# Performance work log

Measured on AMD Instinct MI355X. Metric: run time of the kernel, lower is better.

The kernel has to match this reference:

```python
import jax, jax.numpy as jnp
import numpy as np
import math

B, S, E, H, L, FF = 32, 512, 256, 8, 4, 1024
DH = E // H
EPS = 1e-5


def layernorm(x):
    # nn.LayerNorm(elementwise_affine=False)
    m = jnp.mean(x, axis=-1, keepdims=True)
    v = jnp.mean((x - m) ** 2, axis=-1, keepdims=True)
    return (x - m) / jnp.sqrt(v + EPS)


def make_pos_embedding(e):
    vals = [math.sin(1 / 10000 ** ((i - 1) / e)) if i % 2 == 1
            else math.cos(i / 10000 ** ((i - 1) / e)) for i in range(e)]
    return jnp.asarray(np.array(vals, dtype=np.float32))


def setup_inputs() -> dict:
    key = jax.random.key(0)
    ks = jax.random.split(key, 8)
    sc = 0.02
    x = jax.random.normal(ks[0], (B, S, E), dtype=jnp.float32)
    Wq = jax.random.normal(ks[1], (L, H, DH, DH), dtype=jnp.float32) * sc
    Wk = jax.random.normal(ks[2], (L, H, DH, DH), dtype=jnp.float32) * sc
    Wv = jax.random.normal(ks[3], (L, H, DH, DH), dtype=jnp.float32) * sc
    W1 = jax.random.normal(ks[4], (L, E, FF), dtype=jnp.float32) * sc
    b1 = jnp.zeros((L, FF), dtype=jnp.float32)
    W2 = jax.random.normal(ks[5], (L, FF, E), dtype=jnp.float32) * sc
    b2 = jnp.zeros((L, E), dtype=jnp.float32)
    pos = make_pos_embedding(E)
    return {"x": x, "pos": pos, "Wq": Wq, "Wk": Wk, "Wv": Wv,
            "W1": W1, "b1": b1, "W2": W2, "b2": b2}


def encoder_layer(x, wq, wk, wv, w1, bb1, w2, bb2):
    xn = layernorm(x)
    xh = xn.reshape(B, S, H, DH)  # split embedding into per-head chunks
    q = jnp.einsum('bshd,hde->bhse', xh, wq)
    k = jnp.einsum('bshd,hde->bhse', xh, wk)
    v = jnp.einsum('bshd,hde->bhse', xh, wv)
    scores = jnp.einsum('bhsd,bhtd->bhst', q, k) / jnp.sqrt(jnp.float32(DH))
    a = jax.nn.softmax(scores, axis=-1)
    o = jnp.einsum('bhst,bhtd->bhsd', a, v)
    mha = o.transpose(0, 2, 1, 3).reshape(B, S, E)  # concat heads
    res = mha + x
    rn = layernorm(res)
    ffn = jax.nn.gelu(rn @ w1 + bb1, approximate=False) @ w2 + bb2
    return ffn + res


def reference(x, pos, Wq, Wk, Wv, W1, b1, W2, b2):
    h = x + pos  # fixed sinusoidal positional embedding
    for l in range(L):
        h = encoder_layer(h, Wq[l], Wk[l], Wv[l], W1[l], b1[l], W2[l], b2[l])
    return h
```

## Files before the change

### kernel.cpp

```cpp
#include <hip/hip_runtime.h>
#include <math.h>

#define BB   32
#define SS   512
#define EE   256
#define HH   8
#define LL   4
#define FFD  1024
#define DHD  32

constexpr float LN_EPS = 1e-5f;
constexpr int   NBSE   = BB * SS * EE;

typedef float  f32x4  __attribute__((ext_vector_type(4)));
typedef __bf16 bf16;
typedef __bf16 bf16x4 __attribute__((ext_vector_type(4)));
typedef __bf16 bf16x8 __attribute__((ext_vector_type(8)));

__device__ __forceinline__ void glds16(const bf16* g, bf16* l) {
    __builtin_amdgcn_global_load_lds(
        (const __attribute__((address_space(1))) void*)g,
        (__attribute__((address_space(3))) void*)l,
        16, 0, 0);
}

__device__ __forceinline__ float gelu_f(float x) {
    float u = x * x;
    float t = 1.5957691216057308f * x * (1.0f + 0.044715f * u);
    return x / (1.0f + __expf(-t));
}

__global__ __launch_bounds__(256) void k_cvt_t(const float* __restrict__ in,
                                               bf16* __restrict__ out,
                                               int K, int N) {
    __shared__ float tile[32][33];
    in  += (size_t)blockIdx.z * K * N;
    out += (size_t)blockIdx.z * K * N;
    int n0 = blockIdx.x * 32, k0 = blockIdx.y * 32;
    int tx = threadIdx.x & 31, ty = threadIdx.x >> 5;
    #pragma unroll
    for (int i = 0; i < 32; i += 8)
        tile[ty + i][tx] = in[(size_t)(k0 + ty + i) * N + n0 + tx];
    __syncthreads();
    #pragma unroll
    for (int i = 0; i < 32; i += 8)
        out[(size_t)(n0 + ty + i) * K + k0 + tx] = (bf16)tile[tx][ty + i];
}

__global__ __launch_bounds__(256) void k_cvt_qkv(const float* __restrict__ Wq,
                                                 const float* __restrict__ Wk,
                                                 const float* __restrict__ Wv,
                                                 bf16* __restrict__ Wqt,
                                                 bf16* __restrict__ Wkt,
                                                 bf16* __restrict__ Wvt) {
    __shared__ float tile[32][33];
    int lh = blockIdx.x;
    int z  = blockIdx.y;
    const float* in = (z == 0 ? Wq : z == 1 ? Wk : Wv) + (size_t)lh * 1024;
    bf16* out       = (z == 0 ? Wqt : z == 1 ? Wkt : Wvt) + (size_t)lh * 1024;
    float scale = (z == 0) ? 0.17677669529663687f : 1.0f;
    int tx = threadIdx.x & 31, ty = threadIdx.x >> 5;
    #pragma unroll
    for (int i = 0; i < 32; i += 8)
        tile[ty + i][tx] = in[(ty + i) * 32 + tx];
    __syncthreads();
    #pragma unroll
    for (int i = 0; i < 32; i += 8)
        out[(ty + i) * 32 + tx] = (bf16)(tile[tx][ty + i] * scale);
}

template <bool ADDPOS>
__global__ __launch_bounds__(256) void k_lnqkv(const float* __restrict__ xin,
                                               const float* __restrict__ pos,
                                               float* __restrict__ hout,
                                               const bf16* __restrict__ Wqt,
                                               const bf16* __restrict__ Wkt,
                                               const bf16* __restrict__ Wvt,
                                               bf16* __restrict__ qb,
                                               bf16* __restrict__ kb,
                                               bf16* __restrict__ vb) {
    __shared__ __attribute__((aligned(16))) bf16 Xs[64 * 264];
    int b = blockIdx.x, s0 = blockIdx.y * 64;
    int tid = threadIdx.x, w = tid >> 6, lane = tid & 63;
    size_t rowoff = ((size_t)(b * SS + s0 + w * 16)) * EE + lane * 4;
    const float* hb = xin + rowoff;
    float4 pv;
    if (ADDPOS) pv = *(const float4*)(pos + lane * 4);
    float4 xr[16];
    #pragma unroll
    for (int i = 0; i < 16; i++)
        xr[i] = *(const float4*)(hb + (size_t)i * EE);
    if (ADDPOS) {
        #pragma unroll
        for (int i = 0; i < 16; i++) {
            xr[i].x += pv.x; xr[i].y += pv.y; xr[i].z += pv.z; xr[i].w += pv.w;
            *(float4*)(hout + rowoff + (size_t)i * EE) = xr[i];
        }
    }
    #pragma unroll
    for (int i = 0; i < 16; i++) {
        float4 v4 = xr[i];
        float sum = v4.x + v4.y + v4.z + v4.w;
        #pragma unroll
        for (int m = 1; m <= 32; m <<= 1) sum += __shfl_xor(sum, m, 64);
        float mean = sum * (1.0f / EE);
        float dx = v4.x - mean, dy = v4.y - mean, dz = v4.z - mean, dw = v4.w - mean;
        float ss = dx * dx + dy * dy + dz * dz + dw * dw;
        #pragma unroll
        for (int m = 1; m <= 32; m <<= 1) ss += __shfl_xor(ss, m, 64);
        float rstd = rsqrtf(ss * (1.0f / EE) + LN_EPS);
        bf16x4 o4 = { (bf16)(dx * rstd), (bf16)(dy * rstd), (bf16)(dz * rstd), (bf16)(dw * rstd) };
        *(bf16x4*)&Xs[(w * 16 + i) * 264 + lane * 4] = o4;
    }
    __syncthreads();
    int col = lane & 15, quad = lane >> 4;
    #pragma unroll
    for (int h = 0; h < HH; h++) {
        bf16x8 a = *(const bf16x8*)&Xs[(w * 16 + col) * 264 + h * 32 + quad * 8];
        size_t base = ((size_t)((b * HH + h) * SS) + s0 + w * 16) * DHD;
        #pragma unroll
        for (int nt = 0; nt < 2; nt++) {
            int e = nt * 16 + col;
            bf16x8 bq  = *(const bf16x8*)(Wqt + (h * 32 + e) * 32 + quad * 8);
            bf16x8 bk2 = *(const bf16x8*)(Wkt + (h * 32 + e) * 32 + quad * 8);
            bf16x8 bv2 = *(const bf16x8*)(Wvt + (h * 32 + e) * 32 + quad * 8);
            f32x4 z = {0.f, 0.f, 0.f, 0.f};
            f32x4 cq = __builtin_amdgcn_mfma_f32_16x16x32_bf16(a, bq, z, 0, 0, 0);
            f32x4 ck = __builtin_amdgcn_mfma_f32_16x16x32_bf16(a, bk2, z, 0, 0, 0);
            f32x4 cv = __builtin_amdgcn_mfma_f32_16x16x32_bf16(a, bv2, z, 0, 0, 0);
            #pragma unroll
            for (int r = 0; r < 4; r++) {
                qb[base + (quad * 4 + r) * DHD + e] = (bf16)cq[r];
                kb[base + (quad * 4 + r) * DHD + e] = (bf16)ck[r];
            }
            bf16x4 vv = { (bf16)cv[0], (bf16)cv[1], (bf16)cv[2], (bf16)cv[3] };
            *(bf16x4*)&vb[(((size_t)(b * HH + h)) * DHD + e) * SS + s0 + w * 16 + quad * 4] = vv;
        }
    }
}

#define ATT_LDK 40
#define ATT_LDV 264
#define ATT_LDP 36
__global__ __launch_bounds__(256) void k_attn(const bf16* __restrict__ Q,
                                              const bf16* __restrict__ K,
                                              const bf16* __restrict__ VT,
                                              bf16* __restrict__ O) {
    __shared__ __attribute__((aligned(16))) bf16 Ks[256 * ATT_LDK];
    __shared__ __attribute__((aligned(16))) bf16 Vs[32 * ATT_LDV];
    __shared__ __attribute__((aligned(16))) bf16 Ps[4][16 * ATT_LDP];
    int bh = blockIdx.x;
    int q0 = blockIdx.y * 128;
    int tid = threadIdx.x;
    int w = tid >> 6, lane = tid & 63;
    int col = lane & 15, quad = lane >> 4;
    bf16x8 aq[2];
    #pragma unroll
    for (int sub = 0; sub < 2; sub++)
        aq[sub] = *(const bf16x8*)(Q + ((size_t)(bh * SS + q0 + sub * 64 + w * 16 + col)) * DHD + quad * 8);
    float lr[2] = {0.f, 0.f};
    f32x4 oacc[2][2] = {};
    int ksr = tid >> 2, ksc = (tid & 3) * 8;
    int vd  = tid >> 5, vso = (tid & 31) * 8;
    for (int ph = 0; ph < 2; ph++) {
        int t00 = ph * 256;
        __syncthreads();
        #pragma unroll
        for (int it = 0; it < 4; it++) {
            int rl = it * 64 + ksr;
            *(bf16x8*)&Ks[rl * ATT_LDK + ksc] =
                *(const bf16x8*)(K + ((size_t)(bh * SS + t00 + rl)) * DHD + ksc);
        }
        #pragma unroll
        for (int it = 0; it < 4; it++) {
            int d = it * 8 + vd;
            *(bf16x8*)&Vs[d * ATT_LDV + vso] =
                *(const bf16x8*)(VT + (((size_t)bh * DHD + d) * SS) + t00 + vso);
        }
        __syncthreads();
        #pragma unroll
        for (int i = 0; i < 8; i++) {
            bf16x8 bk[2], bv[2];
            #pragma unroll
            for (int nt = 0; nt < 2; nt++) {
                bk[nt] = *(const bf16x8*)&Ks[(i * 32 + nt * 16 + col) * ATT_LDK + quad * 8];
                bv[nt] = *(const bf16x8*)&Vs[(nt * 16 + col) * ATT_LDV + i * 32 + quad * 8];
            }
            __builtin_amdgcn_s_setprio(1);
            #pragma unroll
            for (int sub = 0; sub < 2; sub++) {
                #pragma unroll
                for (int nt = 0; nt < 2; nt++) {
                    f32x4 z = {0.f, 0.f, 0.f, 0.f};
                    f32x4 st = __builtin_amdgcn_mfma_f32_16x16x32_bf16(bk[nt], aq[sub], z, 0, 0, 0);
                    bf16x4 p4;
                    #pragma unroll
                    for (int r = 0; r < 4; r++) {
                        float p = __expf(st[r]);
                        lr[sub] += p;
                        p4[r] = (bf16)p;
                    }
                    *(bf16x4*)&Ps[w][col * ATT_LDP + nt * 16 + quad * 4] = p4;
                }
                bf16x4 apl = *(const bf16x4*)&Ps[w][col * ATT_LDP + quad * 8];
                bf16x4 aph = *(const bf16x4*)&Ps[w][col * ATT_LDP + quad * 8 + 4];
                bf16x8 ap;
                ap[0] = apl[0]; ap[1] = apl[1]; ap[2] = apl[2]; ap[3] = apl[3];
                ap[4] = aph[0]; ap[5] = aph[1]; ap[6] = aph[2]; ap[7] = aph[3];
                #pragma unroll
                for (int nt = 0; nt < 2; nt++)
                    oacc[sub][nt] = __builtin_amdgcn_mfma_f32_16x16x32_bf16(ap, bv[nt], oacc[sub][nt], 0, 0, 0);
            }
            __builtin_amdgcn_s_setprio(0);
        }
    }
    int b = bh >> 3, hh = bh & 7;
    #pragma unroll
    for (int sub = 0; sub < 2; sub++) {
        float ls = lr[sub];
        ls += __shfl_xor(ls, 16, 64);
        ls += __shfl_xor(ls, 32, 64);
        #pragma unroll
        for (int r = 0; r < 4; r++) {
            float lrow = __shfl(ls, quad * 4 + r, 64);
            float inv = 1.0f / lrow;
            int row = q0 + sub * 64 + w * 16 + quad * 4 + r;
            size_t ob = ((size_t)(b * SS + row)) * EE + hh * 32;
            O[ob + col]      = (bf16)(oacc[sub][0][r] * inv);
            O[ob + 16 + col] = (bf16)(oacc[sub][1][r] * inv);
        }
    }
}

__global__ __launch_bounds__(256, 3) void k_gemm1f(const bf16* __restrict__ ob,
                                                   const float* __restrict__ hb,
                                                   const bf16* __restrict__ Bt,
                                                   const float* __restrict__ bias,
                                                   bf16* __restrict__ C) {
    __shared__ __attribute__((aligned(16))) bf16 As[64 * 256];
    __shared__ __attribute__((aligned(16))) bf16 Bs[256 * 32];
    int tid = threadIdx.x, w = tid >> 6, lane = tid & 63;
    int col = lane & 15, quad = lane >> 4;
    int row0 = blockIdx.x * 64, col0 = blockIdx.y * 256;

    #pragma unroll 4
    for (int rr = 0; rr < 16; rr++) {
        int r = w * 16 + rr;
        size_t g = (size_t)(row0 + r) * EE + lane * 4;
        float4 h4 = *(const float4*)(hb + g);
        bf16x4 o4 = *(const bf16x4*)(ob + g);
        float v0 = h4.x + (float)o4[0], v1 = h4.y + (float)o4[1];
        float v2 = h4.z + (float)o4[2], v3 = h4.w + (float)o4[3];
        float s1 = v0 + v1 + v2 + v3;
        float s2 = v0 * v0 + v1 * v1 + v2 * v2 + v3 * v3;
        #pragma unroll
        for (int m = 1; m <= 32; m <<= 1) {
            s1 += __shfl_xor(s1, m, 64);
            s2 += __shfl_xor(s2, m, 64);
        }
        float mean = s1 * (1.0f / EE);
        float rstd = rsqrtf(s2 * (1.0f / EE) - mean * mean + LN_EPS);
        bf16x4 a4 = { (bf16)((v0 - mean) * rstd), (bf16)((v1 - mean) * rstd),
                      (bf16)((v2 - mean) * rstd), (bf16)((v3 - mean) * rstd) };
        *(bf16x4*)&As[r * 256 + ((lane * 4) ^ ((r & 7) << 3))] = a4;
    }

    int bc = lane >> 2;
    int bp = lane & 3;
    f32x4 acc[4][4] = {};
    for (int k0 = 0; k0 < EE; k0 += 32) {
        __syncthreads();
        #pragma unroll
        for (int i = 0; i < 4; i++) {
            int c = (w * 4 + i) * 16 + bc;
            glds16(Bt + (size_t)(col0 + c) * EE + k0 + ((bp ^ (c & 3)) * 8),
                   &Bs[(w * 4 + i) * 16 * 32]);
        }
        __syncthreads();
        bf16x8 af[4], bf_[4];
        #pragma unroll
        for (int mt = 0; mt < 4; mt++) {
            int r = mt * 16 + col;
            af[mt] = *(const bf16x8*)&As[r * 256 + ((k0 + quad * 8) ^ ((r & 7) << 3))];
        }
        #pragma unroll
        for (int nt = 0; nt < 4; nt++) {
            int c = w * 64 + nt * 16 + col;
            bf_[nt] = *(const bf16x8*)&Bs[c * 32 + ((quad * 8) ^ ((c & 3) << 3))];
        }
        #pragma unroll
        for (int mt = 0; mt < 4; mt++)
            #pragma unroll
            for (int nt = 0; nt < 4; nt++)
                acc[mt][nt] = __builtin_amdgcn_mfma_f32_16x16x32_bf16(bf_[nt], af[mt], acc[mt][nt], 0, 0, 0);
    }
    #pragma unroll
    for (int mt = 0; mt < 4; mt++) {
        int row = row0 + mt * 16 + col;
        #pragma unroll
        for (int nt = 0; nt < 4; nt++) {
            int cc = col0 + w * 64 + nt * 16 + quad * 4;
            float4 b4 = *(const float4*)&bias[cc];
            bf16x4 ov;
            ov[0] = (bf16)gelu_f(acc[mt][nt][0] + b4.x);
            ov[1] = (bf16)gelu_f(acc[mt][nt][1] + b4.y);
            ov[2] = (bf16)gelu_f(acc[mt][nt][2] + b4.z);
            ov[3] = (bf16)gelu_f(acc[mt][nt][3] + b4.w);
            *(bf16x4*)&C[(size_t)row * FFD + cc] = ov;
        }
    }
}

__global__ __launch_bounds__(256) void k_gemm2(const bf16* __restrict__ A,
                                               const bf16* __restrict__ Bt,
                                               const float* __restrict__ bias,
                                               const bf16* __restrict__ ob,
                                               const float* __restrict__ hb,
                                               float* __restrict__ Cf) {
    __shared__ __attribute__((aligned(16))) bf16 As[128 * 64];
    __shared__ __attribute__((aligned(16))) bf16 Bs[64 * 64];
    int tid = threadIdx.x, w = tid >> 6, lane = tid & 63;
    int col = lane & 15, quad = lane >> 4;
    int row0 = blockIdx.x * 128, col0 = blockIdx.y * 64;
    int srow = lane >> 3;
    int spos = lane & 7;
    f32x4 acc[2][4] = {};
    for (int k0 = 0; k0 < FFD; k0 += 64) {
        __syncthreads();
        #pragma unroll
        for (int i = 0; i < 4; i++) {
            int r = (w * 4 + i) * 8 + srow;
            glds16(A + (size_t)(row0 + r) * FFD + k0 + ((spos ^ (r & 7)) * 8),
                   &As[(w * 4 + i) * 8 * 64]);
        }
        #pragma unroll
        for (int i = 0; i < 2; i++) {
            int r = (w * 2 + i) * 8 + srow;
            glds16(Bt + (size_t)(col0 + r) * FFD + k0 + ((spos ^ (r & 7)) * 8),
                   &Bs[(w * 2 + i) * 8 * 64]);
        }
        __syncthreads();
        bf16x8 af[2][2], bf_[4][2];
        #pragma unroll
        for (int mt = 0; mt < 2; mt++) {
            int r = w * 32 + mt * 16 + col;
            #pragma unroll
            for (int kk = 0; kk < 2; kk++)
                af[mt][kk] = *(const bf16x8*)&As[r * 64 + ((kk * 32 + quad * 8) ^ ((r & 7) << 3))];
        }
        #pragma unroll
        for (int nt = 0; nt < 4; nt++) {
            int r = nt * 16 + col;
            #pragma unroll
            for (int kk = 0; kk < 2; kk++)
                bf_[nt][kk] = *(const bf16x8*)&Bs[r * 64 + ((kk * 32 + quad * 8) ^ ((r & 7) << 3))];
        }
        #pragma unroll
        for (int kk = 0; kk < 2; kk++)
            #pragma unroll
            for (int mt = 0; mt < 2; mt++)
                #pragma unroll
                for (int nt = 0; nt < 4; nt++)
                    acc[mt][nt] = __builtin_amdgcn_mfma_f32_16x16x32_bf16(bf_[nt][kk], af[mt][kk], acc[mt][nt], 0, 0, 0);
    }
    #pragma unroll
    for (int mt = 0; mt < 2; mt++) {
        int row = row0 + w * 32 + mt * 16 + col;
        #pragma unroll
        for (int nt = 0; nt < 4; nt++) {
            int cc = col0 + nt * 16 + quad * 4;
            float4 b4 = *(const float4*)&bias[cc];
            float4 h4 = *(const float4*)&hb[(size_t)row * EE + cc];
            bf16x4 o4 = *(const bf16x4*)&ob[(size_t)row * EE + cc];
            float4 out;
            out.x = acc[mt][nt][0] + b4.x + h4.x + (float)o4[0];
            out.y = acc[mt][nt][1] + b4.y + h4.y + (float)o4[1];
            out.z = acc[mt][nt][2] + b4.z + h4.z + (float)o4[2];
            out.w = acc[mt][nt][3] + b4.w + h4.w + (float)o4[3];
            *(float4*)&Cf[(size_t)row * EE + cc] = out;
        }
    }
}

extern "C" void kernel_launch(void* const* d_in, const int* in_sizes, int n_in,
                              void* d_out, int out_size, void* d_ws, size_t ws_size,
                              hipStream_t stream) {
    (void)in_sizes; (void)n_in; (void)out_size; (void)ws_size;
    const float* x   = (const float*)d_in[0];
    const float* pos = (const float*)d_in[1];
    const float* Wq  = (const float*)d_in[2];
    const float* Wk  = (const float*)d_in[3];
    const float* Wv  = (const float*)d_in[4];
    const float* W1  = (const float*)d_in[5];
    const float* b1  = (const float*)d_in[6];
    const float* W2  = (const float*)d_in[7];
    const float* b2  = (const float*)d_in[8];

    float* ws = (float*)d_ws;
    size_t N = (size_t)NBSE;
    float* h  = ws;
    bf16* ob  = (bf16*)(ws + N);
    bf16* qb  = (bf16*)(ws + 2 * N);
    bf16* kb  = qb + N;
    bf16* vb  = kb + N;
    bf16* ffb = (bf16*)(ws + 2 * N);
    bf16* W1t = (bf16*)(ws + 4 * N);
    bf16* W2t = W1t + (size_t)LL * EE * FFD;
    bf16* Wqt = W2t + (size_t)LL * EE * FFD;
    bf16* Wkt = Wqt + (size_t)LL * HH * DHD * DHD;
    bf16* Wvt = Wkt + (size_t)LL * HH * DHD * DHD;

    k_cvt_t<<<dim3(FFD / 32, EE / 32, LL), 256, 0, stream>>>(W1, W1t, EE, FFD);
    k_cvt_t<<<dim3(EE / 32, FFD / 32, LL), 256, 0, stream>>>(W2, W2t, FFD, EE);
    k_cvt_qkv<<<dim3(LL * HH, 3), 256, 0, stream>>>(Wq, Wk, Wv, Wqt, Wkt, Wvt);
    for (int l = 0; l < LL; l++) {
        if (l == 0)
            k_lnqkv<true><<<dim3(BB, SS / 64), 256, 0, stream>>>(
                x, pos, h, Wqt, Wkt, Wvt, qb, kb, vb);
        else
            k_lnqkv<false><<<dim3(BB, SS / 64), 256, 0, stream>>>(
                h, nullptr, nullptr,
                Wqt + (size_t)l * HH * DHD * DHD, Wkt + (size_t)l * HH * DHD * DHD,
                Wvt + (size_t)l * HH * DHD * DHD, qb, kb, vb);
        k_attn<<<dim3(BB * HH, SS / 128), 256, 0, stream>>>(qb, kb, vb, ob);
        k_gemm1f<<<dim3(BB * SS / 64, FFD / 256), 256, 0, stream>>>(
            ob, h, W1t + (size_t)l * FFD * EE, b1 + (size_t)l * FFD, ffb);
        float* outp = (l == LL - 1) ? (float*)d_out : h;
        k_gemm2<<<dim3(BB * SS / 128, EE / 64), 256, 0, stream>>>(
            ffb, W2t + (size_t)l * EE * FFD, b2 + (size_t)l * EE, ob, h, outp);
    }
}
```

Before: 443.1 us.

## Double-buffer GEMM tiles, prefetch attention K/V, merge weight prep, vectorize QKV stores

```diff
diff --git a/kernel.cpp b/kernel.cpp
--- a/kernel.cpp
+++ b/kernel.cpp
@@ -30,43 +30,50 @@
     return x / (1.0f + __expf(-t));
 }
 
-__global__ __launch_bounds__(256) void k_cvt_t(const float* __restrict__ in,
-                                               bf16* __restrict__ out,
-                                               int K, int N) {
+__global__ __launch_bounds__(256) void k_prep(const float* __restrict__ W1,
+                                              const float* __restrict__ W2,
+                                              const float* __restrict__ Wq,
+                                              const float* __restrict__ Wk,
+                                              const float* __restrict__ Wv,
+                                              bf16* __restrict__ W1t,
+                                              bf16* __restrict__ W2t,
+                                              bf16* __restrict__ Wqt,
+                                              bf16* __restrict__ Wkt,
+                                              bf16* __restrict__ Wvt) {
     __shared__ float tile[32][33];
-    in  += (size_t)blockIdx.z * K * N;
-    out += (size_t)blockIdx.z * K * N;
-    int n0 = blockIdx.x * 32, k0 = blockIdx.y * 32;
+    int bid = blockIdx.x;
     int tx = threadIdx.x & 31, ty = threadIdx.x >> 5;
-    #pragma unroll
-    for (int i = 0; i < 32; i += 8)
-        tile[ty + i][tx] = in[(size_t)(k0 + ty + i) * N + n0 + tx];
-    __syncthreads();
-    #pragma unroll
-    for (int i = 0; i < 32; i += 8)
-        out[(size_t)(n0 + ty + i) * K + k0 + tx] = (bf16)tile[tx][ty + i];
-}
-
-__global__ __launch_bounds__(256) void k_cvt_qkv(const float* __restrict__ Wq,
-                                                 const float* __restrict__ Wk,
-                                                 const float* __restrict__ Wv,
-                                                 bf16* __restrict__ Wqt,
-                                                 bf16* __restrict__ Wkt,
-                                                 bf16* __restrict__ Wvt) {
-    __shared__ float tile[32][33];
-    int lh = blockIdx.x;
-    int z  = blockIdx.y;
-    const float* in = (z == 0 ? Wq : z == 1 ? Wk : Wv) + (size_t)lh * 1024;
-    bf16* out       = (z == 0 ? Wqt : z == 1 ? Wkt : Wvt) + (size_t)lh * 1024;
-    float scale = (z == 0) ? 0.17677669529663687f : 1.0f;
-    int tx = threadIdx.x & 31, ty = threadIdx.x >> 5;
-    #pragma unroll
-    for (int i = 0; i < 32; i += 8)
-        tile[ty + i][tx] = in[(ty + i) * 32 + tx];
-    __syncthreads();
-    #pragma unroll
-    for (int i = 0; i < 32; i += 8)
-        out[(ty + i) * 32 + tx] = (bf16)(tile[tx][ty + i] * scale);
+    if (bid < 2048) {
+        bool isw2 = bid >= 1024;
+        int id = isw2 ? bid - 1024 : bid;
+        int K = isw2 ? FFD : EE, N = isw2 ? EE : FFD;
+        int l = id >> 8, rem = id & 255;
+        int n0, k0;
+        if (isw2) { n0 = (rem & 7) * 32;  k0 = (rem >> 3) * 32; }
+        else      { n0 = (rem & 31) * 32; k0 = (rem >> 5) * 32; }
+        const float* in = (isw2 ? W2 : W1) + (size_t)l * K * N;
+        bf16* out       = (isw2 ? W2t : W1t) + (size_t)l * K * N;
+        #pragma unroll
+        for (int i = 0; i < 32; i += 8)
+            tile[ty + i][tx] = in[(size_t)(k0 + ty + i) * N + n0 + tx];
+        __syncthreads();
+        #pragma unroll
+        for (int i = 0; i < 32; i += 8)
+            out[(size_t)(n0 + ty + i) * K + k0 + tx] = (bf16)tile[tx][ty + i];
+    } else {
+        int id = bid - 2048;
+        int lh = id & 31, z = id >> 5;
+        const float* in = (z == 0 ? Wq : z == 1 ? Wk : Wv) + (size_t)lh * 1024;
+        bf16* out       = (z == 0 ? Wqt : z == 1 ? Wkt : Wvt) + (size_t)lh * 1024;
+        float scale = (z == 0) ? 0.17677669529663687f : 1.0f;
+        #pragma unroll
+        for (int i = 0; i < 32; i += 8)
+            tile[ty + i][tx] = in[(ty + i) * 32 + tx];
+        __syncthreads();
+        #pragma unroll
+        for (int i = 0; i < 32; i += 8)
+            out[(ty + i) * 32 + tx] = (bf16)(tile[tx][ty + i] * scale);
+    }
 }
 
 template <bool ADDPOS>
@@ -125,14 +132,14 @@
             bf16x8 bk2 = *(const bf16x8*)(Wkt + (h * 32 + e) * 32 + quad * 8);
             bf16x8 bv2 = *(const bf16x8*)(Wvt + (h * 32 + e) * 32 + quad * 8);
             f32x4 z = {0.f, 0.f, 0.f, 0.f};
-            f32x4 cq = __builtin_amdgcn_mfma_f32_16x16x32_bf16(a, bq, z, 0, 0, 0);
-            f32x4 ck = __builtin_amdgcn_mfma_f32_16x16x32_bf16(a, bk2, z, 0, 0, 0);
+            f32x4 cq = __builtin_amdgcn_mfma_f32_16x16x32_bf16(bq, a, z, 0, 0, 0);
+            f32x4 ck = __builtin_amdgcn_mfma_f32_16x16x32_bf16(bk2, a, z, 0, 0, 0);
             f32x4 cv = __builtin_amdgcn_mfma_f32_16x16x32_bf16(a, bv2, z, 0, 0, 0);
-            #pragma unroll
-            for (int r = 0; r < 4; r++) {
-                qb[base + (quad * 4 + r) * DHD + e] = (bf16)cq[r];
-                kb[base + (quad * 4 + r) * DHD + e] = (bf16)ck[r];
-            }
+            bf16x4 q4 = { (bf16)cq[0], (bf16)cq[1], (bf16)cq[2], (bf16)cq[3] };
+            bf16x4 k4 = { (bf16)ck[0], (bf16)ck[1], (bf16)ck[2], (bf16)ck[3] };
+            size_t tb = base + (size_t)col * DHD + nt * 16 + quad * 4;
+            *(bf16x4*)&qb[tb] = q4;
+            *(bf16x4*)&kb[tb] = k4;
             bf16x4 vv = { (bf16)cv[0], (bf16)cv[1], (bf16)cv[2], (bf16)cv[3] };
             *(bf16x4*)&vb[(((size_t)(b * HH + h)) * DHD + e) * SS + s0 + w * 16 + quad * 4] = vv;
         }
@@ -162,20 +169,25 @@
     f32x4 oacc[2][2] = {};
     int ksr = tid >> 2, ksc = (tid & 3) * 8;
     int vd  = tid >> 5, vso = (tid & 31) * 8;
+    bf16x8 kr[4], vr[4];
+    #pragma unroll
+    for (int it = 0; it < 4; it++) {
+        kr[it] = *(const bf16x8*)(K + ((size_t)(bh * SS + it * 64 + ksr)) * DHD + ksc);
+        vr[it] = *(const bf16x8*)(VT + (((size_t)bh * DHD + it * 8 + vd) * SS) + vso);
+    }
     for (int ph = 0; ph < 2; ph++) {
-        int t00 = ph * 256;
         __syncthreads();
         #pragma unroll
         for (int it = 0; it < 4; it++) {
-            int rl = it * 64 + ksr;
-            *(bf16x8*)&Ks[rl * ATT_LDK + ksc] =
-                *(const bf16x8*)(K + ((size_t)(bh * SS + t00 + rl)) * DHD + ksc);
-        }
-        #pragma unroll
-        for (int it = 0; it < 4; it++) {
-            int d = it * 8 + vd;
-            *(bf16x8*)&Vs[d * ATT_LDV + vso] =
-                *(const bf16x8*)(VT + (((size_t)bh * DHD + d) * SS) + t00 + vso);
+            *(bf16x8*)&Ks[(it * 64 + ksr) * ATT_LDK + ksc] = kr[it];
+            *(bf16x8*)&Vs[(it * 8 + vd) * ATT_LDV + vso] = vr[it];
+        }
+        if (ph == 0) {
+            #pragma unroll
+            for (int it = 0; it < 4; it++) {
+                kr[it] = *(const bf16x8*)(K + ((size_t)(bh * SS + 256 + it * 64 + ksr)) * DHD + ksc);
+                vr[it] = *(const bf16x8*)(VT + (((size_t)bh * DHD + it * 8 + vd) * SS) + 256 + vso);
+            }
         }
         __syncthreads();
         #pragma unroll
@@ -232,13 +244,13 @@
     }
 }
 
-__global__ __launch_bounds__(256, 3) void k_gemm1f(const bf16* __restrict__ ob,
+__global__ __launch_bounds__(256, 2) void k_gemm1f(const bf16* __restrict__ ob,
                                                    const float* __restrict__ hb,
                                                    const bf16* __restrict__ Bt,
                                                    const float* __restrict__ bias,
                                                    bf16* __restrict__ C) {
     __shared__ __attribute__((aligned(16))) bf16 As[64 * 256];
-    __shared__ __attribute__((aligned(16))) bf16 Bs[256 * 32];
+    __shared__ __attribute__((aligned(16))) bf16 Bs[2][256 * 32];
     int tid = threadIdx.x, w = tid >> 6, lane = tid & 63;
     int col = lane & 15, quad = lane >> 4;
     int row0 = blockIdx.x * 64, col0 = blockIdx.y * 256;
@@ -267,16 +279,26 @@
 
     int bc = lane >> 2;
     int bp = lane & 3;
-    f32x4 acc[4][4] = {};
-    for (int k0 = 0; k0 < EE; k0 += 32) {
-        __syncthreads();
+    auto stageB = [&](int buf, int k0) {
         #pragma unroll
         for (int i = 0; i < 4; i++) {
             int c = (w * 4 + i) * 16 + bc;
             glds16(Bt + (size_t)(col0 + c) * EE + k0 + ((bp ^ (c & 3)) * 8),
-                   &Bs[(w * 4 + i) * 16 * 32]);
-        }
-        __syncthreads();
+                   &Bs[buf][(w * 4 + i) * 16 * 32]);
+        }
+    };
+    asm volatile("s_waitcnt lgkmcnt(0)" ::: "memory");
+    stageB(0, 0);
+    f32x4 acc[4][4] = {};
+    for (int t = 0; t < 8; t++) {
+        if (t < 7) {
+            stageB((t + 1) & 1, (t + 1) * 32);
+            asm volatile("s_waitcnt vmcnt(4)" ::: "memory");
+        } else {
+            asm volatile("s_waitcnt vmcnt(0)" ::: "memory");
+        }
+        __builtin_amdgcn_s_barrier();
+        int k0 = t * 32, buf = t & 1;
         bf16x8 af[4], bf_[4];
         #pragma unroll
         for (int mt = 0; mt < 4; mt++) {
@@ -286,13 +308,14 @@
         #pragma unroll
         for (int nt = 0; nt < 4; nt++) {
             int c = w * 64 + nt * 16 + col;
-            bf_[nt] = *(const bf16x8*)&Bs[c * 32 + ((quad * 8) ^ ((c & 3) << 3))];
+            bf_[nt] = *(const bf16x8*)&Bs[buf][c * 32 + ((quad * 8) ^ ((c & 3) << 3))];
         }
         #pragma unroll
         for (int mt = 0; mt < 4; mt++)
             #pragma unroll
             for (int nt = 0; nt < 4; nt++)
                 acc[mt][nt] = __builtin_amdgcn_mfma_f32_16x16x32_bf16(bf_[nt], af[mt], acc[mt][nt], 0, 0, 0);
+        __builtin_amdgcn_s_barrier();
     }
     #pragma unroll
     for (int mt = 0; mt < 4; mt++) {
@@ -311,49 +334,58 @@
     }
 }
 
-__global__ __launch_bounds__(256) void k_gemm2(const bf16* __restrict__ A,
-                                               const bf16* __restrict__ Bt,
-                                               const float* __restrict__ bias,
-                                               const bf16* __restrict__ ob,
-                                               const float* __restrict__ hb,
-                                               float* __restrict__ Cf) {
-    __shared__ __attribute__((aligned(16))) bf16 As[128 * 64];
-    __shared__ __attribute__((aligned(16))) bf16 Bs[64 * 64];
+__global__ __launch_bounds__(256, 3) void k_gemm2(const bf16* __restrict__ A,
+                                                  const bf16* __restrict__ Bt,
+                                                  const float* __restrict__ bias,
+                                                  const bf16* __restrict__ ob,
+                                                  const float* __restrict__ hb,
+                                                  float* __restrict__ Cf) {
+    __shared__ __attribute__((aligned(16))) bf16 As[2][128 * 64];
+    __shared__ __attribute__((aligned(16))) bf16 Bs[2][64 * 64];
     int tid = threadIdx.x, w = tid >> 6, lane = tid & 63;
     int col = lane & 15, quad = lane >> 4;
     int row0 = blockIdx.x * 128, col0 = blockIdx.y * 64;
     int srow = lane >> 3;
     int spos = lane & 7;
-    f32x4 acc[2][4] = {};
-    for (int k0 = 0; k0 < FFD; k0 += 64) {
-        __syncthreads();
+    auto stageAB = [&](int buf, int k0) {
         #pragma unroll
         for (int i = 0; i < 4; i++) {
             int r = (w * 4 + i) * 8 + srow;
             glds16(A + (size_t)(row0 + r) * FFD + k0 + ((spos ^ (r & 7)) * 8),
-                   &As[(w * 4 + i) * 8 * 64]);
+                   &As[buf][(w * 4 + i) * 8 * 64]);
         }
         #pragma unroll
         for (int i = 0; i < 2; i++) {
             int r = (w * 2 + i) * 8 + srow;
             glds16(Bt + (size_t)(col0 + r) * FFD + k0 + ((spos ^ (r & 7)) * 8),
-                   &Bs[(w * 2 + i) * 8 * 64]);
-        }
-        __syncthreads();
+                   &Bs[buf][(w * 2 + i) * 8 * 64]);
+        }
+    };
+    stageAB(0, 0);
+    f32x4 acc[2][4] = {};
+    for (int t = 0; t < 16; t++) {
+        if (t < 15) {
+            stageAB((t + 1) & 1, (t + 1) * 64);
+            asm volatile("s_waitcnt vmcnt(6)" ::: "memory");
+        } else {
+            asm volatile("s_waitcnt vmcnt(0)" ::: "memory");
+        }
+        __builtin_amdgcn_s_barrier();
+        int buf = t & 1;
         bf16x8 af[2][2], bf_[4][2];
         #pragma unroll
         for (int mt = 0; mt < 2; mt++) {
             int r = w * 32 + mt * 16 + col;
             #pragma unroll
             for (int kk = 0; kk < 2; kk++)
-                af[mt][kk] = *(const bf16x8*)&As[r * 64 + ((kk * 32 + quad * 8) ^ ((r & 7) << 3))];
+                af[mt][kk] = *(const bf16x8*)&As[buf][r * 64 + ((kk * 32 + quad * 8) ^ ((r & 7) << 3))];
         }
         #pragma unroll
         for (int nt = 0; nt < 4; nt++) {
             int r = nt * 16 + col;
             #pragma unroll
             for (int kk = 0; kk < 2; kk++)
-                bf_[nt][kk] = *(const bf16x8*)&Bs[r * 64 + ((kk * 32 + quad * 8) ^ ((r & 7) << 3))];
+                bf_[nt][kk] = *(const bf16x8*)&Bs[buf][r * 64 + ((kk * 32 + quad * 8) ^ ((r & 7) << 3))];
         }
         #pragma unroll
         for (int kk = 0; kk < 2; kk++)
@@ -362,6 +394,7 @@
                 #pragma unroll
                 for (int nt = 0; nt < 4; nt++)
                     acc[mt][nt] = __builtin_amdgcn_mfma_f32_16x16x32_bf16(bf_[nt][kk], af[mt][kk], acc[mt][nt], 0, 0, 0);
+        __builtin_amdgcn_s_barrier();
     }
     #pragma unroll
     for (int mt = 0; mt < 2; mt++) {
@@ -410,9 +443,7 @@
     bf16* Wkt = Wqt + (size_t)LL * HH * DHD * DHD;
     bf16* Wvt = Wkt + (size_t)LL * HH * DHD * DHD;
 
-    k_cvt_t<<<dim3(FFD / 32, EE / 32, LL), 256, 0, stream>>>(W1, W1t, EE, FFD);
-    k_cvt_t<<<dim3(EE / 32, FFD / 32, LL), 256, 0, stream>>>(W2, W2t, FFD, EE);
-    k_cvt_qkv<<<dim3(LL * HH, 3), 256, 0, stream>>>(Wq, Wk, Wv, Wqt, Wkt, Wvt);
+    k_prep<<<2144, 256, 0, stream>>>(W1, W2, Wq, Wk, Wv, W1t, W2t, Wqt, Wkt, Wvt);
     for (int l = 0; l < LL; l++) {
         if (l == 0)
             k_lnqkv<true><<<dim3(BB, SS / 64), 256, 0, stream>>>(
```

New measurement: 441.0 us. About the same (-0.5%).
